# Kernel optimization log

Hardware: AMD Instinct MI355X
Metric: run time of the kernel (lower is better)

Reference implementation:

```python
import jax, jax.numpy as jnp
import numpy as np

D = 256
NH = 8
DH = D // NH
DFF = 1024
NLAYER = 6
LIN = 20
HOUT = 10
NEG = -1e9


def _ln(x, s, b, eps=1e-5):
    mu = jnp.mean(x, axis=-1, keepdims=True)
    var = jnp.mean((x - mu) ** 2, axis=-1, keepdims=True)
    return (x - mu) * jax.lax.rsqrt(var + eps) * s + b


def setup_inputs() -> dict:
    key = jax.random.key(0)
    ks = jax.random.split(key, 24)
    B, C, Q = 2, 1536, 512
    sc = 0.02
    inp = {
        'ctx_x': jax.random.normal(ks[0], (B, C, LIN), jnp.float32),
        'ctx_z': jax.random.normal(ks[1], (B, C, HOUT), jnp.float32),
        'qry_x': jax.random.normal(ks[2], (B, Q, LIN), jnp.float32),
        't_ctx': jax.random.randint(ks[3], (B, C), 0, 1024, jnp.int64 if jax.config.jax_enable_x64 else jnp.int32),
        't_qry': jax.random.randint(ks[4], (B, Q), 0, 2048, jnp.int64 if jax.config.jax_enable_x64 else jnp.int32),
        'W_ctx': sc * jax.random.normal(ks[5], (D, LIN + HOUT), jnp.float32),
        'b_ctx': jnp.zeros((D,), jnp.float32),
        'W_qry': sc * jax.random.normal(ks[6], (D, LIN + HOUT), jnp.float32),
        'b_qry': jnp.zeros((D,), jnp.float32),
        'alpha': 0.01 * jnp.ones((NH,), jnp.float32),
        'Wqkv': sc * jax.random.normal(ks[7], (NLAYER, 3 * D, D), jnp.float32),
        'bqkv': jnp.zeros((NLAYER, 3 * D), jnp.float32),
        'Wo': sc * jax.random.normal(ks[8], (NLAYER, D, D), jnp.float32),
        'bo': jnp.zeros((NLAYER, D), jnp.float32),
        'ln1_s': jnp.ones((NLAYER, D), jnp.float32),
        'ln1_b': jnp.zeros((NLAYER, D), jnp.float32),
        'W1': sc * jax.random.normal(ks[9], (NLAYER, DFF, D), jnp.float32),
        'b1': jnp.zeros((NLAYER, DFF), jnp.float32),
        'W2': sc * jax.random.normal(ks[10], (NLAYER, D, DFF), jnp.float32),
        'b2': jnp.zeros((NLAYER, D), jnp.float32),
        'ln2_s': jnp.ones((NLAYER, D), jnp.float32),
        'ln2_b': jnp.zeros((NLAYER, D), jnp.float32),
        'W_out': sc * jax.random.normal(ks[11], (HOUT, D), jnp.float32),
        'b_out': jnp.zeros((HOUT,), jnp.float32),
    }
    return inp


def _forward(ctx_x, ctx_z, qry_x, t_ctx, t_qry, W_ctx, b_ctx, W_qry, b_qry,
             alpha, Wqkv, bqkv, Wo, bo, ln1_s, ln1_b, W1, b1, W2, b2,
             ln2_s, ln2_b, W_out, b_out):
    B, C, _ = ctx_x.shape
    Q = qry_x.shape[1]
    S = C + Q
    ctx_in = jnp.concatenate([ctx_x, ctx_z], axis=-1)               # [B,C,L+H]
    qry_in = jnp.concatenate([qry_x, jnp.zeros((B, Q, HOUT), ctx_x.dtype)], axis=-1)
    Z = jnp.concatenate([ctx_in @ W_ctx.T + b_ctx,
                         qry_in @ W_qry.T + b_qry], axis=1)          # [B,S,d]
    t_all = jnp.concatenate([t_ctx, t_qry], axis=1)                  # [B,S]
    # structural mask: nobody attends to query columns (True = disallowed)
    struct = (jnp.arange(S)[None, :] >= C)                           # [1,S] -> broadcast over rows
    nofuture = t_all[:, :, None] < t_all[:, None, :]                 # [B,S,S]
    mask = struct[None, :, :] | nofuture                             # [B,S,S]
    # learnable per-head recency bias: -alpha_h * |t_i - t_j|
    dist = jnp.abs(t_all[:, :, None] - t_all[:, None, :]).astype(Z.dtype)
    bias = -alpha[None, :, None, None] * dist[:, None, :, :]         # [B,h,S,S]
    scale = 1.0 / np.sqrt(DH)

    for l in range(NLAYER):
        qkv = Z @ Wqkv[l].T + bqkv[l]                                # [B,S,3d]
        q, k, v = jnp.split(qkv, 3, axis=-1)
        q = q.reshape(B, S, NH, DH).transpose(0, 2, 1, 3)            # [B,h,S,dh]
        k = k.reshape(B, S, NH, DH).transpose(0, 2, 1, 3)
        v = v.reshape(B, S, NH, DH).transpose(0, 2, 1, 3)
        scores = jnp.einsum('bhid,bhjd->bhij', q, k) * scale + bias
        scores = jnp.where(mask[:, None, :, :], NEG, scores)
        p = jax.nn.softmax(scores, axis=-1)
        attn = jnp.einsum('bhij,bhjd->bhid', p, v)                   # [B,h,S,dh]
        attn = attn.transpose(0, 2, 1, 3).reshape(B, S, D)
        Z = _ln(Z + attn @ Wo[l].T + bo[l], ln1_s[l], ln1_b[l])
        ff = jax.nn.relu(Z @ W1[l].T + b1[l]) @ W2[l].T + b2[l]
        Z = _ln(Z + ff, ln2_s[l], ln2_b[l])

    return Z[:, C:, :] @ W_out.T + b_out                             # [B,Q,H]


def reference(ctx_x, ctx_z, qry_x, t_ctx, t_qry, W_ctx, b_ctx, W_qry, b_qry,
              alpha, Wqkv, bqkv, Wo, bo, ln1_s, ln1_b, W1, b1, W2, b2,
              ln2_s, ln2_b, W_out, b_out):
    return _forward(ctx_x, ctx_z, qry_x, t_ctx, t_qry, W_ctx, b_ctx, W_qry,
                    b_qry, alpha, Wqkv, bqkv, Wo, bo, ln1_s, ln1_b, W1, b1,
                    W2, b2, ln2_s, ln2_b, W_out, b_out)
```

## Files before the change

### kernel.cpp

```cpp
#include <hip/hip_runtime.h>
#include <hip/hip_bf16.h>
#include <cstddef>

#define BB   2
#define CTX  1536
#define QQ   512
#define S_LEN 2048
#define DD   256
#define NH   8
#define DH   32
#define DFF  1024
#define NL   6
#define LIN  20
#define HOUTD 10
#define KHALF (CTX / 2)

typedef _Float16 f16x2 __attribute__((ext_vector_type(2)));
typedef _Float16 f16x4 __attribute__((ext_vector_type(4)));
typedef _Float16 f16x8 __attribute__((ext_vector_type(8)));
typedef float f32x4 __attribute__((ext_vector_type(4)));

#define N4_QKV (NL * 3 * DD * DD / 4)
#define N4_WO  (NL * DD * DD / 4)
#define N4_W1  (NL * DFF * DD / 4)
#define N4_W2  (NL * DD * DFF / 4)

#define QSCALE (0.17677669529663687f * 1.44269504088896f)

__global__ __launch_bounds__(256) void cvtall_k(
    const float* __restrict__ wqkv, const float* __restrict__ wo,
    const float* __restrict__ w1, const float* __restrict__ w2,
    _Float16* __restrict__ hqkv, _Float16* __restrict__ ho,
    _Float16* __restrict__ h1, _Float16* __restrict__ h2)
{
    int i = blockIdx.x * 256 + threadIdx.x;
    const float* s; _Float16* t; int j = i;
    if (j < N4_QKV) { s = wqkv; t = hqkv; }
    else if ((j -= N4_QKV) < N4_WO) { s = wo; t = ho; }
    else if ((j -= N4_WO) < N4_W1) { s = w1; t = h1; }
    else if ((j -= N4_W1) < N4_W2) { s = w2; t = h2; }
    else return;
    float4 v = ((const float4*)s)[j];
    f16x4 h = {(_Float16)v.x, (_Float16)v.y, (_Float16)v.z, (_Float16)v.w};
    ((f16x4*)t)[j] = h;
}

__global__ __launch_bounds__(256) void embed_k(
    const float* __restrict__ ctx_x, const float* __restrict__ ctx_z,
    const float* __restrict__ qry_x,
    const float* __restrict__ W_ctx, const float* __restrict__ b_ctx,
    const float* __restrict__ W_qry, const float* __restrict__ b_qry,
    const int* __restrict__ t_ctx, const int* __restrict__ t_qry,
    float* __restrict__ Z, _Float16* __restrict__ Zh, float* __restrict__ tf)
{
    int row = blockIdx.x;
    int d = threadIdx.x;
    int b = row >> 11, s = row & (S_LEN - 1);
    float acc;
    if (s < CTX) {
        const float* x1 = ctx_x + (size_t)(b * CTX + s) * LIN;
        const float* x2 = ctx_z + (size_t)(b * CTX + s) * HOUTD;
        const float* w = W_ctx + (size_t)d * (LIN + HOUTD);
        acc = b_ctx[d];
        #pragma unroll
        for (int i = 0; i < LIN; i++) acc += x1[i] * w[i];
        #pragma unroll
        for (int i = 0; i < HOUTD; i++) acc += x2[i] * w[LIN + i];
        if (d == 0) tf[row] = (float)t_ctx[b * CTX + s];
    } else {
        int qi = s - CTX;
        const float* x1 = qry_x + (size_t)(b * QQ + qi) * LIN;
        const float* w = W_qry + (size_t)d * (LIN + HOUTD);
        acc = b_qry[d];
        #pragma unroll
        for (int i = 0; i < LIN; i++) acc += x1[i] * w[i];
        if (d == 0) tf[row] = (float)t_qry[b * QQ + qi];
    }
    Z[(size_t)row * DD + d] = acc;
    Zh[(size_t)row * DD + d] = (_Float16)acc;
}

__global__ __launch_bounds__(256) void hgemm_k(
    const _Float16* __restrict__ X, const _Float16* __restrict__ W,
    const float* __restrict__ bias, float* __restrict__ Y0,
    float* __restrict__ Y1, float* __restrict__ Y2, float* __restrict__ Y3,
    _Float16* __restrict__ Yh,
    int M, int N, int K, int lda, int mode,
    _Float16* __restrict__ Qh, _Float16* __restrict__ Kh, _Float16* __restrict__ Vh)
{
    __shared__ _Float16 Ah[2][64][40];
    __shared__ _Float16 Bh[2][64][40];
    const int tid = threadIdx.x;
    const int bm = blockIdx.x << 6, bn = blockIdx.y << 6;
    const int kbase = blockIdx.z * K;
    const int lr = tid >> 2;
    const int lk = (tid & 3) << 3;
    const int w = tid >> 6, lane = tid & 63;
    const int c = lane & 15, g = lane >> 4;
    const int wm = (w >> 1) << 5, wn = (w & 1) << 5;

    f32x4 acc00 = {0.f,0.f,0.f,0.f}, acc01 = {0.f,0.f,0.f,0.f};
    f32x4 acc10 = {0.f,0.f,0.f,0.f}, acc11 = {0.f,0.f,0.f,0.f};

    const _Float16* Xp = X + (size_t)(bm + lr) * lda + kbase + lk;
    const _Float16* Wp = W + (size_t)(bn + lr) * lda + kbase + lk;

    f16x8 xa = *(const f16x8*)Xp;
    f16x8 wb = *(const f16x8*)Wp;
    const int nt = K >> 5;
    int buf = 0;
    for (int t = 0; t < nt; t++) {
        *(f16x8*)&Ah[buf][lr][lk] = xa;
        *(f16x8*)&Bh[buf][lr][lk] = wb;
        __syncthreads();
        if (t + 1 < nt) {
            xa = *(const f16x8*)(Xp + ((size_t)(t + 1) << 5));
            wb = *(const f16x8*)(Wp + ((size_t)(t + 1) << 5));
        }
        f16x8 a0 = *(const f16x8*)&Ah[buf][wm + c][g << 3];
        f16x8 a1 = *(const f16x8*)&Ah[buf][wm + 16 + c][g << 3];
        f16x8 b0 = *(const f16x8*)&Bh[buf][wn + c][g << 3];
        f16x8 b1 = *(const f16x8*)&Bh[buf][wn + 16 + c][g << 3];
        acc00 = __builtin_amdgcn_mfma_f32_16x16x32_f16(a0, b0, acc00, 0, 0, 0);
        acc01 = __builtin_amdgcn_mfma_f32_16x16x32_f16(a0, b1, acc01, 0, 0, 0);
        acc10 = __builtin_amdgcn_mfma_f32_16x16x32_f16(a1, b0, acc10, 0, 0, 0);
        acc11 = __builtin_amdgcn_mfma_f32_16x16x32_f16(a1, b1, acc11, 0, 0, 0);
        buf ^= 1;
    }

    float* Yt = (blockIdx.z == 0) ? Y0 : (blockIdx.z == 1) ? Y1
              : (blockIdx.z == 2) ? Y2 : Y3;
    f32x4 accs[2][2] = {{acc00, acc01}, {acc10, acc11}};
    #pragma unroll
    for (int fm = 0; fm < 2; fm++) {
        #pragma unroll
        for (int fn = 0; fn < 2; fn++) {
            int colb = bn + wn + (fn << 4) + c;
            float bv = (blockIdx.z == 0) ? bias[colb] : 0.0f;
            if (mode == 2) {
                int which = colb >> 8, h = (colb >> 5) & 7, d = colb & 31;
                int row0 = bm + wm + (fm << 4) + (g << 2);
                int bb2 = row0 >> 11, ss0 = row0 & (S_LEN - 1);
                int bhi = (bb2 << 3) + h;
                if (which == 2) {
                    f16x4 v4 = {(_Float16)(accs[fm][fn][0] + bv),
                                (_Float16)(accs[fm][fn][1] + bv),
                                (_Float16)(accs[fm][fn][2] + bv),
                                (_Float16)(accs[fm][fn][3] + bv)};
                    *(f16x4*)(Vh + ((size_t)bhi * DH + d) * S_LEN + ss0) = v4;
                } else {
                    #pragma unroll
                    for (int r = 0; r < 4; r++) {
                        float v = accs[fm][fn][r] + bv;
                        if (which == 0)
                            Qh[((size_t)bhi * S_LEN + ss0 + r) * DH + d] = (_Float16)(v * QSCALE);
                        else
                            Kh[((size_t)bhi * S_LEN + ss0 + r) * DH + d] = (_Float16)v;
                    }
                }
            } else {
                #pragma unroll
                for (int r = 0; r < 4; r++) {
                    int row = bm + wm + (fm << 4) + (g << 2) + r;
                    float v = accs[fm][fn][r] + bv;
                    if (mode == 0) {
                        Yt[(size_t)row * N + colb] = v;
                    } else {
                        Yh[(size_t)row * N + colb] = (_Float16)fmaxf(v, 0.0f);
                    }
                }
            }
        }
    }
}

__global__ __launch_bounds__(256) void gemmln_k(
    const _Float16* __restrict__ X, const _Float16* __restrict__ W,
    const float* __restrict__ bias, float* __restrict__ Z,
    _Float16* __restrict__ Zh, const float* __restrict__ sw,
    const float* __restrict__ bw)
{
    __shared__ _Float16 Ast[2][16][40];
    __shared__ _Float16 Bst[2][256][40];
    __shared__ float lred[4][16][2];
    const int tid = threadIdx.x;
    const int bm = blockIdx.x << 4;
    const int w = tid >> 6, lane = tid & 63;
    const int c = lane & 15, g = lane >> 4;
    const int br = tid >> 2, bk = (tid & 3) << 3;

    f32x4 acc[4] = {};
    const _Float16* Wp = W + (size_t)br * DD + bk;
    f16x8 p0 = *(const f16x8*)Wp;
    f16x8 p1 = *(const f16x8*)(Wp + (size_t)64 * DD);
    f16x8 p2 = *(const f16x8*)(Wp + (size_t)128 * DD);
    f16x8 p3 = *(const f16x8*)(Wp + (size_t)192 * DD);
    f16x8 xa;
    if (tid < 64) xa = *(const f16x8*)(X + (size_t)(bm + br) * DD + bk);
    int buf = 0;
    #pragma unroll
    for (int t = 0; t < 8; t++) {
        if (tid < 64) *(f16x8*)&Ast[buf][br][bk] = xa;
        *(f16x8*)&Bst[buf][br][bk] = p0;
        *(f16x8*)&Bst[buf][br + 64][bk] = p1;
        *(f16x8*)&Bst[buf][br + 128][bk] = p2;
        *(f16x8*)&Bst[buf][br + 192][bk] = p3;
        __syncthreads();
        if (t < 7) {
            int o = (t + 1) << 5;
            if (tid < 64) xa = *(const f16x8*)(X + (size_t)(bm + br) * DD + o + bk);
            p0 = *(const f16x8*)(Wp + o);
            p1 = *(const f16x8*)(Wp + (size_t)64 * DD + o);
            p2 = *(const f16x8*)(Wp + (size_t)128 * DD + o);
            p3 = *(const f16x8*)(Wp + (size_t)192 * DD + o);
        }
        f16x8 a = *(const f16x8*)&Ast[buf][c][g << 3];
        #pragma unroll
        for (int f = 0; f < 4; f++) {
            f16x8 bfr = *(const f16x8*)&Bst[buf][(w << 6) + (f << 4) + c][g << 3];
            acc[f] = __builtin_amdgcn_mfma_f32_16x16x32_f16(a, bfr, acc[f], 0, 0, 0);
        }
        buf ^= 1;
    }

    float vals[4][4];
    float s1[4] = {0.f,0.f,0.f,0.f}, s2[4] = {0.f,0.f,0.f,0.f};
    #pragma unroll
    for (int f = 0; f < 4; f++) {
        int col = (w << 6) + (f << 4) + c;
        float bv = bias[col];
        #pragma unroll
        for (int r = 0; r < 4; r++) {
            int row = bm + (g << 2) + r;
            float v = acc[f][r] + bv + Z[(size_t)row * DD + col];
            vals[f][r] = v; s1[r] += v; s2[r] += v * v;
        }
    }
    #pragma unroll
    for (int off = 1; off < 16; off <<= 1) {
        #pragma unroll
        for (int r = 0; r < 4; r++) {
            s1[r] += __shfl_xor(s1[r], off, 64);
            s2[r] += __shfl_xor(s2[r], off, 64);
        }
    }
    if (c == 0) {
        #pragma unroll
        for (int r = 0; r < 4; r++) {
            lred[w][(g << 2) + r][0] = s1[r];
            lred[w][(g << 2) + r][1] = s2[r];
        }
    }
    __syncthreads();
    float mu_r[4], rs_r[4];
    #pragma unroll
    for (int r = 0; r < 4; r++) {
        int lr_ = (g << 2) + r;
        float S1 = lred[0][lr_][0] + lred[1][lr_][0] + lred[2][lr_][0] + lred[3][lr_][0];
        float S2 = lred[0][lr_][1] + lred[1][lr_][1] + lred[2][lr_][1] + lred[3][lr_][1];
        float mu = S1 * (1.0f / 256.0f);
        float var = S2 * (1.0f / 256.0f) - mu * mu;
        mu_r[r] = mu; rs_r[r] = rsqrtf(var + 1e-5f);
    }
    #pragma unroll
    for (int f = 0; f < 4; f++) {
        int col = (w << 6) + (f << 4) + c;
        float swv = sw[col], bwv = bw[col];
        #pragma unroll
        for (int r = 0; r < 4; r++) {
            int row = bm + (g << 2) + r;
            float o = (vals[f][r] - mu_r[r]) * rs_r[r] * swv + bwv;
            Z[(size_t)row * DD + col] = o;
            Zh[(size_t)row * DD + col] = (_Float16)o;
        }
    }
}

__global__ __launch_bounds__(256) void ln4_k(
    float* __restrict__ Z, const float* __restrict__ Y0,
    const float* __restrict__ Y1, const float* __restrict__ Y2,
    const float* __restrict__ Y3,
    const float* __restrict__ sw, const float* __restrict__ bw,
    _Float16* __restrict__ Zh)
{
    const int w = threadIdx.x >> 6, lane = threadIdx.x & 63;
    const int row = (blockIdx.x << 2) + w;
    float4 z = ((const float4*)(Z + (size_t)row * DD))[lane];
    float4 y0 = ((const float4*)(Y0 + (size_t)row * DD))[lane];
    float4 y1 = ((const float4*)(Y1 + (size_t)row * DD))[lane];
    float4 y2 = ((const float4*)(Y2 + (size_t)row * DD))[lane];
    float4 y3 = ((const float4*)(Y3 + (size_t)row * DD))[lane];
    float x0 = z.x + (y0.x + y1.x) + (y2.x + y3.x);
    float x1 = z.y + (y0.y + y1.y) + (y2.y + y3.y);
    float x2 = z.z + (y0.z + y1.z) + (y2.z + y3.z);
    float x3 = z.w + (y0.w + y1.w) + (y2.w + y3.w);
    float s1 = (x0 + x1) + (x2 + x3);
    float s2 = (x0 * x0 + x1 * x1) + (x2 * x2 + x3 * x3);
    #pragma unroll
    for (int off = 1; off < 64; off <<= 1) {
        s1 += __shfl_xor(s1, off, 64);
        s2 += __shfl_xor(s2, off, 64);
    }
    float mu = s1 * (1.0f / 256.0f);
    float var = s2 * (1.0f / 256.0f) - mu * mu;
    float rs = rsqrtf(var + 1e-5f);
    float4 sv = ((const float4*)sw)[lane];
    float4 bv = ((const float4*)bw)[lane];
    float o0 = (x0 - mu) * rs * sv.x + bv.x;
    float o1 = (x1 - mu) * rs * sv.y + bv.y;
    float o2 = (x2 - mu) * rs * sv.z + bv.z;
    float o3 = (x3 - mu) * rs * sv.w + bv.w;
    ((float4*)(Z + (size_t)row * DD))[lane] = make_float4(o0, o1, o2, o3);
    f16x4 oh = {(_Float16)o0, (_Float16)o1, (_Float16)o2, (_Float16)o3};
    ((f16x4*)(Zh + (size_t)row * DD))[lane] = oh;
}

__global__ __launch_bounds__(256) void ln4qo_k(
    const float* __restrict__ Z, const float* __restrict__ Y0,
    const float* __restrict__ Y1, const float* __restrict__ Y2,
    const float* __restrict__ Y3,
    const float* __restrict__ sw, const float* __restrict__ bw,
    const float* __restrict__ Wout, const float* __restrict__ bout,
    float* __restrict__ out)
{
    const int w = threadIdx.x >> 6, lane = threadIdx.x & 63;
    const int qrow = (blockIdx.x << 2) + w;
    const int b = qrow >> 9;
    const int row = b * S_LEN + CTX + (qrow & (QQ - 1));
    float4 z = ((const float4*)(Z + (size_t)row * DD))[lane];
    float4 y0 = ((const float4*)(Y0 + (size_t)row * DD))[lane];
    float4 y1 = ((const float4*)(Y1 + (size_t)row * DD))[lane];
    float4 y2 = ((const float4*)(Y2 + (size_t)row * DD))[lane];
    float4 y3 = ((const float4*)(Y3 + (size_t)row * DD))[lane];
    float x0 = z.x + (y0.x + y1.x) + (y2.x + y3.x);
    float x1 = z.y + (y0.y + y1.y) + (y2.y + y3.y);
    float x2 = z.z + (y0.z + y1.z) + (y2.z + y3.z);
    float x3 = z.w + (y0.w + y1.w) + (y2.w + y3.w);
    float s1 = (x0 + x1) + (x2 + x3);
    float s2 = (x0 * x0 + x1 * x1) + (x2 * x2 + x3 * x3);
    #pragma unroll
    for (int off = 1; off < 64; off <<= 1) {
        s1 += __shfl_xor(s1, off, 64);
        s2 += __shfl_xor(s2, off, 64);
    }
    float mu = s1 * (1.0f / 256.0f);
    float var = s2 * (1.0f / 256.0f) - mu * mu;
    float rs = rsqrtf(var + 1e-5f);
    float4 sv = ((const float4*)sw)[lane];
    float4 bv = ((const float4*)bw)[lane];
    float o0 = (x0 - mu) * rs * sv.x + bv.x;
    float o1 = (x1 - mu) * rs * sv.y + bv.y;
    float o2 = (x2 - mu) * rs * sv.z + bv.z;
    float o3 = (x3 - mu) * rs * sv.w + bv.w;
    #pragma unroll
    for (int ho = 0; ho < HOUTD; ho++) {
        float4 wv = ((const float4*)(Wout + (size_t)ho * DD))[lane];
        float s = (o0 * wv.x + o1 * wv.y) + (o2 * wv.z + o3 * wv.w);
        #pragma unroll
        for (int off = 1; off < 64; off <<= 1) s += __shfl_xor(s, off, 64);
        if (lane == ho) out[(size_t)qrow * HOUTD + ho] = s + bout[ho];
    }
}

__global__ __launch_bounds__(1024, 4) void attn_k(
    const _Float16* __restrict__ Qf, const _Float16* __restrict__ Kf,
    const _Float16* __restrict__ Vf, const float* __restrict__ tf_all,
    const float* __restrict__ alpha, _Float16* __restrict__ O)
{
    const int bh = blockIdx.x >> 4;
    const int itile = blockIdx.x & 15;
    const int b = bh >> 3, h = bh & 7;
    const int tid = threadIdx.x;
    const int w16 = tid >> 6;
    const int wg = w16 >> 3;
    const int wq = w16 & 7;
    const int ltid = tid & 511;
    const int lane = tid & 63;
    const int c = lane & 15, g = lane >> 4;
    const int i0 = (itile << 7) + (wq << 4);
    const int jbase = wg * KHALF;

    __shared__ __align__(16) char smem[92160];
    _Float16 (*Kl)[2][128][40] = (_Float16(*)[2][128][40])smem;
    _Float16 (*Vl)[2][32][136] = (_Float16(*)[2][32][136])(smem + 40960);
    float* tbl = (float*)(smem + 75776);
    float* ptl = (float*)(smem + 83968);
    float (*sacc)[16][36] = (float(*)[16][36])smem;
    float (*sml)[2][16] = (float(*)[2][16])(smem + 36864);

    const float LOG2E = 1.44269504088896f;
    const float ah2 = alpha[h] * LOG2E;

    const _Float16* Qbh = Qf + (size_t)bh * S_LEN * DH;
    const _Float16* Kbh = Kf + (size_t)bh * S_LEN * DH;
    const _Float16* Vbh = Vf + (size_t)bh * DH * S_LEN;
    const float* tb = tf_all + b * S_LEN;

    f16x8 qfrag = *(const f16x8*)(Qbh + (size_t)(i0 + c) * DH + (g << 3));
    const float ti = tb[i0 + c];

    const int kr = ltid >> 2, kc = (ltid & 3) << 3;
    const int vr = ltid >> 4, vc = (ltid & 15) << 3;

    {
        float t0 = tb[tid], t1 = tb[tid + 1024];
        tbl[tid] = t0; tbl[tid + 1024] = t1;
        ptl[tid] = ah2 * t0; ptl[tid + 1024] = ah2 * t1;
    }

    float m2 = -3.0e38f, l = 0.0f;
    f32x4 acc0 = {0.f, 0.f, 0.f, 0.f};
    f32x4 acc1 = {0.f, 0.f, 0.f, 0.f};
    const f32x4 zero = {0.f, 0.f, 0.f, 0.f};

    f16x8 kpre = *(const f16x8*)(Kbh + (size_t)(jbase + kr) * DH + kc);
    f16x8 vpre = *(const f16x8*)(Vbh + (size_t)vr * S_LEN + jbase + vc);
    int buf = 0;

    for (int kt = 0; kt < KHALF; kt += 128) {
        *(f16x8*)&Kl[wg][buf][kr][kc] = kpre;
        *(f16x8*)&Vl[wg][buf][vr][vc] = vpre;
        __syncthreads();
        if (kt + 128 < KHALF) {
            kpre = *(const f16x8*)(Kbh + (size_t)(jbase + kt + 128 + kr) * DH + kc);
            vpre = *(const f16x8*)(Vbh + (size_t)vr * S_LEN + jbase + kt + 128 + vc);
        }
        #pragma unroll
        for (int jj = 0; jj < 128; jj += 32) {
            const int j0 = jbase + kt + jj;
            f16x8 kf0 = *(const f16x8*)&Kl[wg][buf][jj + c][g << 3];
            f16x8 kf1 = *(const f16x8*)&Kl[wg][buf][jj + 16 + c][g << 3];
            __builtin_amdgcn_s_setprio(1);
            f32x4 dA = __builtin_amdgcn_mfma_f32_16x16x32_f16(kf0, qfrag, zero, 0, 0, 0);
            f32x4 dB = __builtin_amdgcn_mfma_f32_16x16x32_f16(kf1, qfrag, zero, 0, 0, 0);
            __builtin_amdgcn_s_setprio(0);
            float4 tjA = *(const float4*)&tbl[j0 + (g << 2)];
            float4 tjB = *(const float4*)&tbl[j0 + 16 + (g << 2)];
            float4 ptA = *(const float4*)&ptl[j0 + (g << 2)];
            float4 ptB = *(const float4*)&ptl[j0 + 16 + (g << 2)];
            float sA0 = (tjA.x <= ti) ? dA[0] + ptA.x : -1e9f;
            float sA1 = (tjA.y <= ti) ? dA[1] + ptA.y : -1e9f;
            float sA2 = (tjA.z <= ti) ? dA[2] + ptA.z : -1e9f;
            float sA3 = (tjA.w <= ti) ? dA[3] + ptA.w : -1e9f;
            float sB0 = (tjB.x <= ti) ? dB[0] + ptB.x : -1e9f;
            float sB1 = (tjB.y <= ti) ? dB[1] + ptB.y : -1e9f;
            float sB2 = (tjB.z <= ti) ? dB[2] + ptB.z : -1e9f;
            float sB3 = (tjB.w <= ti) ? dB[3] + ptB.w : -1e9f;
            float pmaxl = fmaxf(fmaxf(fmaxf(sA0, sA1), fmaxf(sA2, sA3)),
                                fmaxf(fmaxf(sB0, sB1), fmaxf(sB2, sB3)));
            if (__any(pmaxl > m2 + 8.0f)) {
                float pm = fmaxf(pmaxl, __shfl_xor(pmaxl, 16, 64));
                pm = fmaxf(pm, __shfl_xor(pm, 32, 64));
                float mnew = fmaxf(m2, pm);
                float fsc = __builtin_amdgcn_exp2f(m2 - mnew);
                m2 = mnew;
                l *= fsc; acc0 *= fsc; acc1 *= fsc;
            }
            float pA0 = __builtin_amdgcn_exp2f(sA0 - m2);
            float pA1 = __builtin_amdgcn_exp2f(sA1 - m2);
            float pA2 = __builtin_amdgcn_exp2f(sA2 - m2);
            float pA3 = __builtin_amdgcn_exp2f(sA3 - m2);
            float pB0 = __builtin_amdgcn_exp2f(sB0 - m2);
            float pB1 = __builtin_amdgcn_exp2f(sB1 - m2);
            float pB2 = __builtin_amdgcn_exp2f(sB2 - m2);
            float pB3 = __builtin_amdgcn_exp2f(sB3 - m2);
            l += ((pA0 + pA1) + (pA2 + pA3)) + ((pB0 + pB1) + (pB2 + pB3));
            f16x4 pfA = {(_Float16)pA0, (_Float16)pA1, (_Float16)pA2, (_Float16)pA3};
            f16x4 pfB = {(_Float16)pB0, (_Float16)pB1, (_Float16)pB2, (_Float16)pB3};
            f16x4 vA0 = *(const f16x4*)&Vl[wg][buf][c][jj + (g << 2)];
            f16x4 vA1 = *(const f16x4*)&Vl[wg][buf][16 + c][jj + (g << 2)];
            f16x4 vB0 = *(const f16x4*)&Vl[wg][buf][c][jj + 16 + (g << 2)];
            f16x4 vB1 = *(const f16x4*)&Vl[wg][buf][16 + c][jj + 16 + (g << 2)];
            __builtin_amdgcn_s_setprio(1);
            acc0 = __builtin_amdgcn_mfma_f32_16x16x16f16(vA0, pfA, acc0, 0, 0, 0);
            acc0 = __builtin_amdgcn_mfma_f32_16x16x16f16(vB0, pfB, acc0, 0, 0, 0);
            acc1 = __builtin_amdgcn_mfma_f32_16x16x16f16(vA1, pfA, acc1, 0, 0, 0);
            acc1 = __builtin_amdgcn_mfma_f32_16x16x16f16(vB1, pfB, acc1, 0, 0, 0);
            __builtin_amdgcn_s_setprio(0);
        }
        buf ^= 1;
    }

    l += __shfl_xor(l, 16, 64);
    l += __shfl_xor(l, 32, 64);

    __syncthreads();
    *(f32x4*)&sacc[w16][c][g << 2] = acc0;
    *(f32x4*)&sacc[w16][c][16 + (g << 2)] = acc1;
    if (g == 0) { sml[w16][0][c] = m2; sml[w16][1][c] = l; }
    __syncthreads();

    {
        const int qt = tid >> 7;
        const int q = (tid >> 3) & 15;
        const int dh0 = (tid & 7) << 2;
        float m0 = sml[qt][0][q], m1 = sml[qt + 8][0][q];
        float M = fmaxf(m0, m1);
        float f0 = __builtin_amdgcn_exp2f(m0 - M);
        float f1 = __builtin_amdgcn_exp2f(m1 - M);
        float L = sml[qt][1][q] * f0 + sml[qt + 8][1][q] * f1;
        float a0 = sacc[qt][q][dh0 + 0] * f0 + sacc[qt + 8][q][dh0 + 0] * f1;
        float a1 = sacc[qt][q][dh0 + 1] * f0 + sacc[qt + 8][q][dh0 + 1] * f1;
        float a2 = sacc[qt][q][dh0 + 2] * f0 + sacc[qt + 8][q][dh0 + 2] * f1;
        float a3 = sacc[qt][q][dh0 + 3] * f0 + sacc[qt + 8][q][dh0 + 3] * f1;
        if (M < -4.9e8f) {
            float vs0 = 0.f, vs1 = 0.f, vs2 = 0.f, vs3 = 0.f;
            const _Float16* vp = Vbh + (size_t)dh0 * S_LEN + CTX;
            for (int j = 0; j < QQ; j += 8) {
                f16x8 x0 = *(const f16x8*)(vp + j);
                f16x8 x1 = *(const f16x8*)(vp + S_LEN + j);
                f16x8 x2 = *(const f16x8*)(vp + 2 * S_LEN + j);
                f16x8 x3 = *(const f16x8*)(vp + 3 * S_LEN + j);
                #pragma unroll
                for (int e = 0; e < 8; e++) {
                    vs0 += (float)x0[e]; vs1 += (float)x1[e];
                    vs2 += (float)x2[e]; vs3 += (float)x3[e];
                }
            }
            a0 += vs0; a1 += vs1; a2 += vs2; a3 += vs3;
            L += (float)QQ;
        }
        float inv = 1.0f / L;
        int row = b * S_LEN + (itile << 7) + (qt << 4) + q;
        f16x4 o = {(_Float16)(a0 * inv), (_Float16)(a1 * inv),
                   (_Float16)(a2 * inv), (_Float16)(a3 * inv)};
        *(f16x4*)(O + (size_t)row * DD + h * DH + dh0) = o;
    }
}

extern "C" void kernel_launch(void* const* d_in, const int* in_sizes, int n_in,
                              void* d_out, int out_size, void* d_ws, size_t ws_size,
                              hipStream_t stream) {
    (void)in_sizes; (void)n_in; (void)out_size; (void)ws_size;
    const float* ctx_x = (const float*)d_in[0];
    const float* ctx_z = (const float*)d_in[1];
    const float* qry_x = (const float*)d_in[2];
    const int* t_ctx = (const int*)d_in[3];
    const int* t_qry = (const int*)d_in[4];
    const float* W_ctx = (const float*)d_in[5];
    const float* b_ctx = (const float*)d_in[6];
    const float* W_qry = (const float*)d_in[7];
    const float* b_qry = (const float*)d_in[8];
    const float* alpha = (const float*)d_in[9];
    const float* Wqkv = (const float*)d_in[10];
    const float* bqkv = (const float*)d_in[11];
    const float* Wo = (const float*)d_in[12];
    const float* bo = (const float*)d_in[13];
    const float* ln1_s = (const float*)d_in[14];
    const float* ln1_b = (const float*)d_in[15];
    const float* W1 = (const float*)d_in[16];
    const float* b1 = (const float*)d_in[17];
    const float* W2 = (const float*)d_in[18];
    const float* b2 = (const float*)d_in[19];
    const float* ln2_s = (const float*)d_in[20];
    const float* ln2_b = (const float*)d_in[21];
    const float* W_out = (const float*)d_in[22];
    const float* b_out = (const float*)d_in[23];

    float* ws = (float*)d_ws;
    const size_t MTOT = (size_t)BB * S_LEN;
    const size_t ZSZ = MTOT * DD;
    float* Z   = ws;
    float* Yb  = ws + ZSZ;
    _Float16* Zh   = (_Float16*)(ws + 2 * ZSZ);
    _Float16* AYh  = (_Float16*)(ws + 2 * ZSZ + ZSZ / 2);
    _Float16* FF1h = (_Float16*)(ws + 3 * ZSZ);
    _Float16* Qh   = (_Float16*)(ws + 5 * ZSZ);
    _Float16* Kh   = (_Float16*)(ws + 5 * ZSZ + ZSZ / 2);
    _Float16* Vh   = (_Float16*)(ws + 6 * ZSZ);
    float* tf_all  = ws + 6 * ZSZ + ZSZ / 2;
    _Float16* Whqkv = (_Float16*)(ws + 6 * ZSZ + ZSZ / 2 + 4096);
    _Float16* Who   = Whqkv + (size_t)NL * 3 * DD * DD;
    _Float16* Wh1   = Who   + (size_t)NL * DD * DD;
    _Float16* Wh2   = Wh1   + (size_t)NL * DFF * DD;
    float* Yb1 = ws + 9 * ZSZ;
    float* Yb2 = ws + 10 * ZSZ;
    float* Yb3 = ws + 11 * ZSZ;

    {
        int n4tot = N4_QKV + N4_WO + N4_W1 + N4_W2;
        cvtall_k<<<(n4tot + 255) / 256, 256, 0, stream>>>(
            Wqkv, Wo, W1, W2, Whqkv, Who, Wh1, Wh2);
    }

    embed_k<<<MTOT, 256, 0, stream>>>(ctx_x, ctx_z, qry_x, W_ctx, b_ctx, W_qry, b_qry,
                                      t_ctx, t_qry, Z, Zh, tf_all);

    for (int l = 0; l < NL; l++) {
        hgemm_k<<<dim3(MTOT / 64, (3 * DD) / 64, 1), 256, 0, stream>>>(
            Zh, Whqkv + (size_t)l * 3 * DD * DD, bqkv + (size_t)l * 3 * DD,
            nullptr, nullptr, nullptr, nullptr, nullptr,
            (int)MTOT, 3 * DD, DD, DD, 2, Qh, Kh, Vh);
        attn_k<<<BB * NH * (S_LEN / 128), 1024, 0, stream>>>(
            Qh, Kh, Vh, tf_all, alpha, AYh);
        gemmln_k<<<MTOT / 16, 256, 0, stream>>>(
            AYh, Who + (size_t)l * DD * DD, bo + (size_t)l * DD,
            Z, Zh, ln1_s + (size_t)l * DD, ln1_b + (size_t)l * DD);
        hgemm_k<<<dim3(MTOT / 64, DFF / 64, 1), 256, 0, stream>>>(
            Zh, Wh1 + (size_t)l * DFF * DD, b1 + (size_t)l * DFF,
            nullptr, nullptr, nullptr, nullptr, FF1h,
            (int)MTOT, DFF, DD, DD, 1, nullptr, nullptr, nullptr);
        hgemm_k<<<dim3(MTOT / 64, DD / 64, 4), 256, 0, stream>>>(
            FF1h, Wh2 + (size_t)l * DD * DFF, b2 + (size_t)l * DD,
            Yb, Yb1, Yb2, Yb3, nullptr,
            (int)MTOT, DD, DFF / 4, DFF, 0, nullptr, nullptr, nullptr);
        if (l < NL - 1) {
            ln4_k<<<MTOT / 4, 256, 0, stream>>>(
                Z, Yb, Yb1, Yb2, Yb3,
                ln2_s + (size_t)l * DD, ln2_b + (size_t)l * DD, Zh);
        } else {
            ln4qo_k<<<(BB * QQ) / 4, 256, 0, stream>>>(
                Z, Yb, Yb1, Yb2, Yb3,
                ln2_s + (size_t)l * DD, ln2_b + (size_t)l * DD,
                W_out, b_out, (float*)d_out);
        }
    }
}
```

Measured before the change: 368.5 us.

## Restrict last-layer attention, Wo and FFN to query rows only

In the final layer only query-row outputs are consumed, so attention, the Wo+LayerNorm GEMM and both FFN GEMMs are launched only over the query rows, with a row remap into the full sequence buffers. The QKV projection still runs over all rows because keys and values for the context are needed. This removes dead computation on context rows in the last layer at the cost of extra index arithmetic and kernel parameters.

```diff
diff --git a/kernel.cpp b/kernel.cpp
--- a/kernel.cpp
+++ b/kernel.cpp
@@ -26,6 +26,10 @@
 #define N4_W2  (NL * DD * DFF / 4)
 
 #define QSCALE (0.17677669529663687f * 1.44269504088896f)
+
+__device__ __forceinline__ int qremap(int r) {
+    return (r >> 9) * S_LEN + CTX + (r & (QQ - 1));
+}
 
 __global__ __launch_bounds__(256) void cvtall_k(
     const float* __restrict__ wqkv, const float* __restrict__ wo,
@@ -85,7 +89,7 @@
     const float* __restrict__ bias, float* __restrict__ Y0,
     float* __restrict__ Y1, float* __restrict__ Y2, float* __restrict__ Y3,
     _Float16* __restrict__ Yh,
-    int M, int N, int K, int lda, int mode,
+    int M, int N, int K, int lda, int mode, int xmap,
     _Float16* __restrict__ Qh, _Float16* __restrict__ Kh, _Float16* __restrict__ Vh)
 {
     __shared__ _Float16 Ah[2][64][40];
@@ -102,7 +106,9 @@
     f32x4 acc00 = {0.f,0.f,0.f,0.f}, acc01 = {0.f,0.f,0.f,0.f};
     f32x4 acc10 = {0.f,0.f,0.f,0.f}, acc11 = {0.f,0.f,0.f,0.f};
 
-    const _Float16* Xp = X + (size_t)(bm + lr) * lda + kbase + lk;
+    int xr = bm + lr;
+    if (xmap) xr = qremap(xr);
+    const _Float16* Xp = X + (size_t)xr * lda + kbase + lk;
     const _Float16* Wp = W + (size_t)(bn + lr) * lda + kbase + lk;
 
     f16x8 xa = *(const f16x8*)Xp;
@@ -178,7 +184,7 @@
     const _Float16* __restrict__ X, const _Float16* __restrict__ W,
     const float* __restrict__ bias, float* __restrict__ Z,
     _Float16* __restrict__ Zh, const float* __restrict__ sw,
-    const float* __restrict__ bw)
+    const float* __restrict__ bw, int qmap)
 {
     __shared__ _Float16 Ast[2][16][40];
     __shared__ _Float16 Bst[2][256][40];
@@ -196,7 +202,9 @@
     f16x8 p2 = *(const f16x8*)(Wp + (size_t)128 * DD);
     f16x8 p3 = *(const f16x8*)(Wp + (size_t)192 * DD);
     f16x8 xa;
-    if (tid < 64) xa = *(const f16x8*)(X + (size_t)(bm + br) * DD + bk);
+    int arow = bm + br;
+    if (qmap) arow = qremap(arow);
+    if (tid < 64) xa = *(const f16x8*)(X + (size_t)arow * DD + bk);
     int buf = 0;
     #pragma unroll
     for (int t = 0; t < 8; t++) {
@@ -208,7 +216,7 @@
         __syncthreads();
         if (t < 7) {
             int o = (t + 1) << 5;
-            if (tid < 64) xa = *(const f16x8*)(X + (size_t)(bm + br) * DD + o + bk);
+            if (tid < 64) xa = *(const f16x8*)(X + (size_t)arow * DD + o + bk);
             p0 = *(const f16x8*)(Wp + o);
             p1 = *(const f16x8*)(Wp + (size_t)64 * DD + o);
             p2 = *(const f16x8*)(Wp + (size_t)128 * DD + o);
@@ -225,14 +233,19 @@
 
     float vals[4][4];
     float s1[4] = {0.f,0.f,0.f,0.f}, s2[4] = {0.f,0.f,0.f,0.f};
+    int rows[4];
+    #pragma unroll
+    for (int r = 0; r < 4; r++) {
+        int row = bm + (g << 2) + r;
+        rows[r] = qmap ? qremap(row) : row;
+    }
     #pragma unroll
     for (int f = 0; f < 4; f++) {
         int col = (w << 6) + (f << 4) + c;
         float bv = bias[col];
         #pragma unroll
         for (int r = 0; r < 4; r++) {
-            int row = bm + (g << 2) + r;
-            float v = acc[f][r] + bv + Z[(size_t)row * DD + col];
+            float v = acc[f][r] + bv + Z[(size_t)rows[r] * DD + col];
             vals[f][r] = v; s1[r] += v; s2[r] += v * v;
         }
     }
@@ -268,10 +281,9 @@
         float swv = sw[col], bwv = bw[col];
         #pragma unroll
         for (int r = 0; r < 4; r++) {
-            int row = bm + (g << 2) + r;
             float o = (vals[f][r] - mu_r[r]) * rs_r[r] * swv + bwv;
-            Z[(size_t)row * DD + col] = o;
-            Zh[(size_t)row * DD + col] = (_Float16)o;
+            Z[(size_t)rows[r] * DD + col] = o;
+            Zh[(size_t)rows[r] * DD + col] = (_Float16)o;
         }
     }
 }
@@ -325,13 +337,12 @@
 {
     const int w = threadIdx.x >> 6, lane = threadIdx.x & 63;
     const int qrow = (blockIdx.x << 2) + w;
-    const int b = qrow >> 9;
-    const int row = b * S_LEN + CTX + (qrow & (QQ - 1));
+    const int row = qremap(qrow);
     float4 z = ((const float4*)(Z + (size_t)row * DD))[lane];
-    float4 y0 = ((const float4*)(Y0 + (size_t)row * DD))[lane];
-    float4 y1 = ((const float4*)(Y1 + (size_t)row * DD))[lane];
-    float4 y2 = ((const float4*)(Y2 + (size_t)row * DD))[lane];
-    float4 y3 = ((const float4*)(Y3 + (size_t)row * DD))[lane];
+    float4 y0 = ((const float4*)(Y0 + (size_t)qrow * DD))[lane];
+    float4 y1 = ((const float4*)(Y1 + (size_t)qrow * DD))[lane];
+    float4 y2 = ((const float4*)(Y2 + (size_t)qrow * DD))[lane];
+    float4 y3 = ((const float4*)(Y3 + (size_t)qrow * DD))[lane];
     float x0 = z.x + (y0.x + y1.x) + (y2.x + y3.x);
     float x1 = z.y + (y0.y + y1.y) + (y2.y + y3.y);
     float x2 = z.z + (y0.z + y1.z) + (y2.z + y3.z);
@@ -365,10 +376,11 @@
 __global__ __launch_bounds__(1024, 4) void attn_k(
     const _Float16* __restrict__ Qf, const _Float16* __restrict__ Kf,
     const _Float16* __restrict__ Vf, const float* __restrict__ tf_all,
-    const float* __restrict__ alpha, _Float16* __restrict__ O)
+    const float* __restrict__ alpha, _Float16* __restrict__ O,
+    int tshift, int ibase)
 {
-    const int bh = blockIdx.x >> 4;
-    const int itile = blockIdx.x & 15;
+    const int bh = blockIdx.x >> tshift;
+    const int itile = blockIdx.x & ((1 << tshift) - 1);
     const int b = bh >> 3, h = bh & 7;
     const int tid = threadIdx.x;
     const int w16 = tid >> 6;
@@ -377,7 +389,7 @@
     const int ltid = tid & 511;
     const int lane = tid & 63;
     const int c = lane & 15, g = lane >> 4;
-    const int i0 = (itile << 7) + (wq << 4);
+    const int i0 = ibase + (itile << 7) + (wq << 4);
     const int jbase = wg * KHALF;
 
     __shared__ __align__(16) char smem[92160];
@@ -521,7 +533,7 @@
             L += (float)QQ;
         }
         float inv = 1.0f / L;
-        int row = b * S_LEN + (itile << 7) + (qt << 4) + q;
+        int row = b * S_LEN + ibase + (itile << 7) + (qt << 4) + q;
         f16x4 o = {(_Float16)(a0 * inv), (_Float16)(a1 * inv),
                    (_Float16)(a2 * inv), (_Float16)(a3 * inv)};
         *(f16x4*)(O + (size_t)row * DD + h * DH + dh0) = o;
@@ -587,24 +599,31 @@
                                       t_ctx, t_qry, Z, Zh, tf_all);
 
     for (int l = 0; l < NL; l++) {
+        const bool last = (l == NL - 1);
+        const int Mff = last ? (BB * QQ) : (int)MTOT;
         hgemm_k<<<dim3(MTOT / 64, (3 * DD) / 64, 1), 256, 0, stream>>>(
             Zh, Whqkv + (size_t)l * 3 * DD * DD, bqkv + (size_t)l * 3 * DD,
             nullptr, nullptr, nullptr, nullptr, nullptr,
-            (int)MTOT, 3 * DD, DD, DD, 2, Qh, Kh, Vh);
-        attn_k<<<BB * NH * (S_LEN / 128), 1024, 0, stream>>>(
-            Qh, Kh, Vh, tf_all, alpha, AYh);
-        gemmln_k<<<MTOT / 16, 256, 0, stream>>>(
+            (int)MTOT, 3 * DD, DD, DD, 2, 0, Qh, Kh, Vh);
+        if (!last) {
+            attn_k<<<BB * NH * (S_LEN / 128), 1024, 0, stream>>>(
+                Qh, Kh, Vh, tf_all, alpha, AYh, 4, 0);
+        } else {
+            attn_k<<<BB * NH * (QQ / 128), 1024, 0, stream>>>(
+                Qh, Kh, Vh, tf_all, alpha, AYh, 2, CTX);
+        }
+        gemmln_k<<<Mff / 16, 256, 0, stream>>>(
             AYh, Who + (size_t)l * DD * DD, bo + (size_t)l * DD,
-            Z, Zh, ln1_s + (size_t)l * DD, ln1_b + (size_t)l * DD);
-        hgemm_k<<<dim3(MTOT / 64, DFF / 64, 1), 256, 0, stream>>>(
+            Z, Zh, ln1_s + (size_t)l * DD, ln1_b + (size_t)l * DD, last ? 1 : 0);
+        hgemm_k<<<dim3(Mff / 64, DFF / 64, 1), 256, 0, stream>>>(
             Zh, Wh1 + (size_t)l * DFF * DD, b1 + (size_t)l * DFF,
             nullptr, nullptr, nullptr, nullptr, FF1h,
-            (int)MTOT, DFF, DD, DD, 1, nullptr, nullptr, nullptr);
-        hgemm_k<<<dim3(MTOT / 64, DD / 64, 4), 256, 0, stream>>>(
+            Mff, DFF, DD, DD, 1, last ? 1 : 0, nullptr, nullptr, nullptr);
+        hgemm_k<<<dim3(Mff / 64, DD / 64, 4), 256, 0, stream>>>(
             FF1h, Wh2 + (size_t)l * DD * DFF, b2 + (size_t)l * DD,
             Yb, Yb1, Yb2, Yb3, nullptr,
-            (int)MTOT, DD, DFF / 4, DFF, 0, nullptr, nullptr, nullptr);
-        if (l < NL - 1) {
+            Mff, DD, DFF / 4, DFF, 0, 0, nullptr, nullptr, nullptr);
+        if (!last) {
             ln4_k<<<MTOT / 4, 256, 0, stream>>>(
                 Z, Yb, Yb1, Yb2, Yb3,
                 ln2_s + (size_t)l * DD, ln2_b + (size_t)l * DD, Zh);
```

After: 361.3 us, median of 2. -2.0%, faster.
